# Optimization experiments

Measured on AMD Instinct MI355X. Metric: run time of the kernel, lower is better.

## Reference

```python
import jax, jax.numpy as jnp
import numpy as np

B_, L_, D_MODEL = 2, 2048, 2048
EXPAND = 2
D_IN = EXPAND * D_MODEL            # 4096 intermediate_size
HEADS = 64
HEAD_DIM = D_IN // HEADS           # 64
STATE = 128
NGROUPS = 1
K = 4                              # conv kernel
CONV_DIM = D_IN + 2 * NGROUPS * STATE   # 4352
PROJ = D_IN + CONV_DIM + HEADS          # 8512
CHUNK = 256
EPS = 1e-5


def setup_inputs() -> dict:
    key = jax.random.key(0)
    ks = jax.random.split(key, 4)
    return {
        "hidden_states": jax.random.normal(ks[0], (B_, L_, D_MODEL), jnp.float32),
        "in_proj_w": jax.random.normal(ks[1], (PROJ, D_MODEL), jnp.float32) * 0.02,
        "conv_w": jax.random.normal(ks[2], (CONV_DIM, K), jnp.float32) * 0.2,
        "conv_b": jnp.zeros((CONV_DIM,), jnp.float32),
        "dt_bias": jnp.ones((HEADS,), jnp.float32),
        "A_log": jnp.log(jnp.arange(1, HEADS + 1, dtype=jnp.float32)),
        "D": jnp.ones((HEADS,), jnp.float32),
        "norm_w": jnp.ones((D_IN,), jnp.float32),
        "out_proj_w": jax.random.normal(ks[3], (D_MODEL, D_IN), jnp.float32) * 0.02,
    }


def _segsum(x):
    # x: [..., T] -> lower-triangular segment sums [..., T, T]
    T = x.shape[-1]
    c = jnp.cumsum(x, axis=-1)
    seg = c[..., :, None] - c[..., None, :]
    return jnp.where(jnp.tril(jnp.ones((T, T), bool)), seg, -jnp.inf)


def _ssd(x, dA, Bm, Cm):
    # chunked SSD scan (exact math of the sequential selective scan)
    # x: [b,l,h,p] (already * dt), dA: [b,l,h], Bm/Cm: [b,l,g,n]
    b, l, h, p = x.shape
    n = Bm.shape[-1]
    c = l // CHUNK
    rep = h // Bm.shape[2]
    Bh = jnp.repeat(Bm, rep, axis=2).reshape(b, c, CHUNK, h, n)
    Ch = jnp.repeat(Cm, rep, axis=2).reshape(b, c, CHUNK, h, n)
    x = x.reshape(b, c, CHUNK, h, p)
    dA = dA.reshape(b, c, CHUNK, h).transpose(0, 3, 1, 2)       # [b,h,c,cl]
    dA_cum = jnp.cumsum(dA, axis=-1)
    Lmat = jnp.exp(_segsum(dA))                                  # [b,h,c,cl,cl]
    # intra-chunk (diagonal) contribution
    Y_diag = jnp.einsum('bcthn,bcshn,bhcts,bcshp->bcthp', Ch, Bh, Lmat, x)
    # per-chunk final states
    decay_states = jnp.exp(dA_cum[..., -1:] - dA_cum)            # [b,h,c,cl]
    states = jnp.einsum('bcshn,bhcs,bcshp->bchpn', Bh, decay_states, x)
    # inter-chunk recurrence
    chunk_decay = jnp.exp(_segsum(jnp.pad(dA_cum[..., -1], ((0, 0), (0, 0), (1, 0)))))  # [b,h,c+1,c+1]
    states = jnp.concatenate([jnp.zeros_like(states[:, :1]), states], axis=1)
    prev = jnp.einsum('bhzc,bchpn->bzhpn', chunk_decay, states)[:, :-1]  # state entering each chunk
    Y_off = jnp.einsum('bcthn,bchpn,bhct->bcthp', Ch, prev, jnp.exp(dA_cum))
    return (Y_diag + Y_off).reshape(b, l, h, p)


def reference(hidden_states, in_proj_w, conv_w, conv_b, dt_bias, A_log, D, norm_w, out_proj_w):
    b, l, _ = hidden_states.shape
    proj = hidden_states @ in_proj_w.T                     # [b,l,PROJ]
    gate = proj[..., :D_IN]
    xBC = proj[..., D_IN:D_IN + CONV_DIM]
    dt = proj[..., D_IN + CONV_DIM:]                       # [b,l,H]
    # causal depthwise conv1d (padding=K-1, truncated to seq_len) + silu
    xp = jnp.pad(xBC, ((0, 0), (K - 1, 0), (0, 0)))
    conv = conv_b + sum(conv_w[:, i] * xp[:, i:i + l, :] for i in range(K))
    xBC = jax.nn.silu(conv)
    x = xBC[..., :D_IN].reshape(b, l, HEADS, HEAD_DIM)
    Bm = xBC[..., D_IN:D_IN + NGROUPS * STATE].reshape(b, l, NGROUPS, STATE)
    Cm = xBC[..., D_IN + NGROUPS * STATE:].reshape(b, l, NGROUPS, STATE)
    dt = jax.nn.softplus(dt + dt_bias)                     # time_step_limit=(0,inf): no clamp
    A = -jnp.exp(A_log)                                    # [H]
    y = _ssd(x * dt[..., None], dt * A, Bm, Cm)            # [b,l,H,P]
    y = y + D[None, None, :, None] * x                     # skip term D*x
    y = y.reshape(b, l, D_IN)
    # MambaRMSNormGated: gate then rms-normalize
    hg = y * jax.nn.silu(gate)
    var = jnp.mean(hg * hg, axis=-1, keepdims=True)
    y = hg * jax.lax.rsqrt(var + EPS) * norm_w
    return y @ out_proj_w.T
```

## Files before the change

kernel.cpp:

```cpp
#include <hip/hip_runtime.h>
#include <hip/hip_bf16.h>
#include <cstdio>

#define LQ 2048
#define BB 2
#define BL 4096
#define DMODEL 2048
#define DIN 4096
#define NH 64
#define HD 64
#define NST 128
#define CONVD 4352
#define PROJD 8512
#define PROJ_PAD2 8704
#define PXW 4416
#define CHK 256
#define NCH 8

typedef __attribute__((ext_vector_type(8))) short short8;
typedef __attribute__((ext_vector_type(4))) float f32x4;

__device__ __forceinline__ unsigned short f2bu(float x) {
  __hip_bfloat16 h = __float2bfloat16(x);
  return __builtin_bit_cast(unsigned short, h);
}

__device__ __forceinline__ f32x4 mfma16(short8 a, short8 b, f32x4 c) {
  return __builtin_amdgcn_mfma_f32_16x16x32_bf16(a, b, c, 0, 0, 0);
}

#define GLD16(gptr, lptr)                                                  \
  __builtin_amdgcn_global_load_lds(                                        \
      (const __attribute__((address_space(1))) void*)(gptr),               \
      (__attribute__((address_space(3))) void*)(lptr), 16, 0, 0)

__global__ void k_cast3(const float* __restrict__ s0, unsigned short* __restrict__ d0,
                        long n0,
                        const float* __restrict__ s1, unsigned short* __restrict__ d1,
                        long n1r, long n1t,
                        const float* __restrict__ s2, unsigned short* __restrict__ d2,
                        long n2) {
  const long ntot8 = (n0 + n1t + n2) >> 3;
  long i = (long)blockIdx.x * blockDim.x + threadIdx.x;
  const long stride = (long)gridDim.x * blockDim.x;
  for (; i < ntot8; i += stride) {
    const long e = i << 3;
    const float* src;
    unsigned short* dst;
    long rel, nreal;
    if (e < n0) { src = s0; dst = d0; rel = e; nreal = n0; }
    else if (e < n0 + n1t) { src = s1; dst = d1; rel = e - n0; nreal = n1r; }
    else { src = s2; dst = d2; rel = e - n0 - n1t; nreal = n2; }
    short8 pk;
    if (rel + 8 <= nreal) {
      const f32x4* sp = reinterpret_cast<const f32x4*>(src + rel);
      f32x4 v0 = sp[0], v1 = sp[1];
#pragma unroll
      for (int u = 0; u < 4; u++) {
        pk[u] = (short)f2bu(v0[u]);
        pk[4 + u] = (short)f2bu(v1[u]);
      }
    } else {
#pragma unroll
      for (int u = 0; u < 8; u++)
        pk[u] = (rel + u < nreal) ? (short)f2bu(src[rel + u]) : (short)0;
    }
    *reinterpret_cast<short8*>(dst + rel) = pk;
  }
}

__device__ __forceinline__ short8 rdfrag(const unsigned short (*mp)[64], int rowbase,
                                         int lane, int kh) {
  const int row = rowbase + (lane & 15);
  const int cg = (((kh << 2) + (lane >> 4)) ^ (lane & 7)) << 3;
  return *reinterpret_cast<const short8*>(&mp[row][cg]);
}

template <bool SPLIT>
__global__ __launch_bounds__(512) void k_gemm256(
    const unsigned short* __restrict__ A, const unsigned short* __restrict__ Bw,
    float* __restrict__ C, unsigned short* __restrict__ gateb,
    float* __restrict__ projx, int Nreal, int K) {
  __shared__ unsigned short sh[2][2][256][64];
  const int tid = threadIdx.x;
  const int lane = tid & 63, w = tid >> 6;
  const int wm = w >> 2, wn2 = w & 3;
  const int gx = gridDim.x;
  const int nwg = gx * gridDim.y;
  const int bid = blockIdx.y * gx + blockIdx.x;
  const int qq = nwg >> 3;
  const int swz = (bid & 7) * qq + (bid >> 3);
  const int m0 = (swz / gx) * 256, n0 = (swz % gx) * 256;
  const int srow = tid >> 3;
  const int sdst = (tid & 7) * 8;
  const int ssrc = ((tid & 7) ^ ((tid >> 3) & 7)) * 8;
  const unsigned short* Ab = A + (size_t)m0 * K;
  const unsigned short* Bb = Bw + (size_t)n0 * K;

#define ST(bf, mt, MP, r0, kk)                                             \
  GLD16(MP + (size_t)((r0) + srow) * K + (kk) + ssrc,                      \
        &sh[bf][mt][(r0) + srow][sdst])

  f32x4 acc[8][4] = {};
  const int nt = K >> 6;

  ST(0, 0, Ab, 0, 0);   ST(0, 0, Ab, 128, 0);
  ST(0, 1, Bb, 0, 0);   ST(0, 1, Bb, 64, 0);
  ST(0, 1, Bb, 128, 0); ST(0, 1, Bb, 192, 0);
  ST(0, 0, Ab, 64, 0);  ST(0, 0, Ab, 192, 0);

#define DO_PHASE(P)                                                        \
  {                                                                        \
    const int rb = wm * 128 + (P) * 32;                                    \
    short8 a00 = rdfrag(sh[cur][0], rb, lane, 0);                          \
    short8 a01 = rdfrag(sh[cur][0], rb, lane, 1);                          \
    short8 a10 = rdfrag(sh[cur][0], rb + 16, lane, 0);                     \
    short8 a11 = rdfrag(sh[cur][0], rb + 16, lane, 1);                     \
    __builtin_amdgcn_s_setprio(1);                                         \
    _Pragma("unroll")                                                      \
    for (int nf = 0; nf < 4; nf++) {                                       \
      acc[2 * (P)][nf] = mfma16(a00, bfr[nf][0], acc[2 * (P)][nf]);        \
      acc[2 * (P)][nf] = mfma16(a01, bfr[nf][1], acc[2 * (P)][nf]);        \
      acc[2 * (P) + 1][nf] = mfma16(a10, bfr[nf][0], acc[2 * (P) + 1][nf]);\
      acc[2 * (P) + 1][nf] = mfma16(a11, bfr[nf][1], acc[2 * (P) + 1][nf]);\
    }                                                                      \
    __builtin_amdgcn_s_setprio(0);                                         \
  }

  for (int t = 0; t < nt; ++t) {
    const int cur = t & 1, nxt = cur ^ 1;
    const int kbn = (t + 1) << 6;
    const bool more = (t + 1 < nt);
    asm volatile("s_waitcnt vmcnt(2)" ::: "memory");
    __builtin_amdgcn_s_barrier();
    if (more) { ST(nxt, 0, Ab, 0, kbn); ST(nxt, 0, Ab, 128, kbn); }
    short8 bfr[4][2];
#pragma unroll
    for (int nf = 0; nf < 4; nf++) {
      bfr[nf][0] = rdfrag(sh[cur][1], wn2 * 64 + nf * 16, lane, 0);
      bfr[nf][1] = rdfrag(sh[cur][1], wn2 * 64 + nf * 16, lane, 1);
    }
    DO_PHASE(0)
    __builtin_amdgcn_s_barrier();
    if (more) { ST(nxt, 1, Bb, 0, kbn); ST(nxt, 1, Bb, 64, kbn); }
    DO_PHASE(1)
    if (more) asm volatile("s_waitcnt vmcnt(4)" ::: "memory");
    else      asm volatile("s_waitcnt vmcnt(0)" ::: "memory");
    __builtin_amdgcn_s_barrier();
    if (more) { ST(nxt, 1, Bb, 128, kbn); ST(nxt, 1, Bb, 192, kbn); }
    DO_PHASE(2)
    __builtin_amdgcn_s_barrier();
    if (more) { ST(nxt, 0, Ab, 64, kbn); ST(nxt, 0, Ab, 192, kbn); }
    DO_PHASE(3)
  }
#undef DO_PHASE
#undef ST

#pragma unroll
  for (int mf = 0; mf < 8; mf++) {
    const int row = m0 + wm * 128 + mf * 16 + ((lane >> 4) << 2);
#pragma unroll
    for (int nf = 0; nf < 4; nf++) {
      const int col = n0 + wn2 * 64 + nf * 16 + (lane & 15);
      if (SPLIT) {
        if (col < DIN) {
#pragma unroll
          for (int v = 0; v < 4; v++)
            gateb[(size_t)(row + v) * DIN + col] = f2bu(acc[mf][nf][v]);
        } else if (col < PROJD) {
#pragma unroll
          for (int v = 0; v < 4; v++)
            projx[(size_t)(row + v) * PXW + (col - DIN)] = acc[mf][nf][v];
        }
      } else {
        if (col < Nreal) {
#pragma unroll
          for (int v = 0; v < 4; v++)
            C[(size_t)(row + v) * Nreal + col] = acc[mf][nf][v];
        }
      }
    }
  }
}

__global__ __launch_bounds__(256) void k_gemm_bt(
    const unsigned short* __restrict__ A, const unsigned short* __restrict__ Bw,
    float* __restrict__ C, int Nreal, int K) {
  __shared__ unsigned short lA[128][64];
  __shared__ unsigned short lB[128][64];
  const int tid = threadIdx.x;
  const int lane = tid & 63, w = tid >> 6;
  const int gx = gridDim.x;
  const int nwg = gx * gridDim.y;
  const int bid = blockIdx.y * gx + blockIdx.x;
  const int qq = nwg >> 3;
  const int swz = (bid & 7) * qq + (bid >> 3);
  const int m0 = (swz / gx) * 128, n0 = (swz % gx) * 128;
  const int wr = (w >> 1) * 64, wc = (w & 1) * 64;
  const int sr = tid >> 3;
  const int sdst = (tid & 7) * 8;
  const int ssrc = ((tid & 7) ^ ((tid >> 3) & 7)) * 8;
  f32x4 acc[4][4] = {};
  for (int kb = 0; kb < K; kb += 64) {
#pragma unroll
    for (int i = 0; i < 4; i++) {
      const int r = sr + i * 32;
      GLD16(A + (size_t)(m0 + r) * K + kb + ssrc, &lA[r][sdst]);
      GLD16(Bw + (size_t)(n0 + r) * K + kb + ssrc, &lB[r][sdst]);
    }
    __syncthreads();
#pragma unroll
    for (int kk = 0; kk < 64; kk += 32) {
      short8 af[4], bf[4];
      const int cg = ((((kk >> 3) + (lane >> 4)) ^ (lane & 7)) << 3);
#pragma unroll
      for (int i = 0; i < 4; i++) {
        af[i] = *reinterpret_cast<const short8*>(&lA[wr + i * 16 + (lane & 15)][cg]);
        bf[i] = *reinterpret_cast<const short8*>(&lB[wc + i * 16 + (lane & 15)][cg]);
      }
#pragma unroll
      for (int mi = 0; mi < 4; mi++)
#pragma unroll
        for (int ni = 0; ni < 4; ni++)
          acc[mi][ni] = mfma16(af[mi], bf[ni], acc[mi][ni]);
    }
    __syncthreads();
  }
#pragma unroll
  for (int mi = 0; mi < 4; mi++) {
    const int row = m0 + wr + mi * 16 + ((lane >> 4) << 2);
#pragma unroll
    for (int ni = 0; ni < 4; ni++) {
      const int col = n0 + wc + ni * 16 + (lane & 15);
      if (col < Nreal) {
#pragma unroll
        for (int v = 0; v < 4; v++)
          C[(size_t)(row + v) * Nreal + col] = acc[mi][ni][v];
      }
    }
  }
}

__global__ __launch_bounds__(256) void k_conv_silu(
    const float* __restrict__ projx, const float* __restrict__ cw,
    const float* __restrict__ cb, float* __restrict__ xbc) {
  const int ch = blockIdx.x * 256 + threadIdx.x;
  const int bt = blockIdx.y;
  const int b = bt >> 11, t = bt & 2047;
  float acc = cb[ch];
#pragma unroll
  for (int i = 0; i < 4; i++) {
    int tt = t - 3 + i;
    if (tt >= 0)
      acc += cw[ch * 4 + i] * projx[((size_t)b * LQ + tt) * PXW + ch];
  }
  float o = acc / (1.f + __expf(-acc));
  xbc[(size_t)bt * CONVD + ch] = o;
}

__global__ __launch_bounds__(256) void k_dt(
    const float* __restrict__ projx, const float* __restrict__ dtb,
    const float* __restrict__ alog, float* __restrict__ dtv,
    float* __restrict__ dac) {
  const int bc = blockIdx.x;
  const int b = bc >> 3, c = bc & 7;
  const int h = threadIdx.x & 63, q = threadIdx.x >> 6;
  const float bias = dtb[h];
  const float Ah = -__expf(alog[h]);
  const size_t base = (size_t)b * LQ + c * CHK + q * 64;
  float vals[64];
  float part = 0.f;
#pragma unroll
  for (int j = 0; j < 64; j++) {
    float raw = projx[(base + j) * PXW + CONVD + h] + bias;
    float dt = raw > 20.f ? raw : log1pf(__expf(raw));
    vals[j] = dt;
    dtv[(base + j) * NH + h] = dt;
    part += dt;
  }
  __shared__ float partials[4][64];
  partials[q][h] = part;
  __syncthreads();
  float cum = 0.f;
  for (int qq = 0; qq < q; qq++) cum += partials[qq][h];
  cum *= Ah;
#pragma unroll
  for (int j = 0; j < 64; j++) {
    cum += vals[j] * Ah;
    dac[(base + j) * NH + h] = cum;
  }
}

__global__ __launch_bounds__(256) void k_cb(const float* __restrict__ xbc,
                                            float* __restrict__ cbuf) {
  const int q = blockIdx.x;
  const int bc = blockIdx.y;
  const int b = bc >> 3, c = bc & 7;
  const int qt = q >> 1, qs = q & 1;
  __shared__ unsigned short lC[128][136];
  __shared__ unsigned short lB[128][136];
  const int tid = threadIdx.x, lane = tid & 63, w = tid >> 6;
  {
    int r = tid >> 1, hf = tid & 1;
    size_t rowc = (size_t)b * LQ + c * CHK + qt * 128 + r;
    size_t rowb = (size_t)b * LQ + c * CHK + qs * 128 + r;
    const f32x4* crp = reinterpret_cast<const f32x4*>(
        xbc + rowc * CONVD + DIN + NST + hf * 64);
    const f32x4* brp = reinterpret_cast<const f32x4*>(
        xbc + rowb * CONVD + DIN + hf * 64);
#pragma unroll
    for (int n4 = 0; n4 < 16; n4++) {
      f32x4 vc = crp[n4], vb = brp[n4];
#pragma unroll
      for (int u = 0; u < 4; u++) {
        lC[r][hf * 64 + n4 * 4 + u] = f2bu(vc[u]);
        lB[r][hf * 64 + n4 * 4 + u] = f2bu(vb[u]);
      }
    }
  }
  __syncthreads();
  const int wr = (w >> 1) * 64, wc = (w & 1) * 64;
  f32x4 acc[4][4] = {};
#pragma unroll
  for (int kk = 0; kk < 128; kk += 32) {
    short8 a[4], bb[4];
    const int ko = kk + ((lane >> 4) << 3);
#pragma unroll
    for (int i = 0; i < 4; i++) {
      a[i] = *reinterpret_cast<const short8*>(&lC[wr + i * 16 + (lane & 15)][ko]);
      bb[i] = *reinterpret_cast<const short8*>(&lB[wc + i * 16 + (lane & 15)][ko]);
    }
#pragma unroll
    for (int mi = 0; mi < 4; mi++)
#pragma unroll
      for (int ni = 0; ni < 4; ni++)
        acc[mi][ni] = mfma16(a[mi], bb[ni], acc[mi][ni]);
  }
  float* outp = cbuf + (size_t)bc * (CHK * CHK);
#pragma unroll
  for (int mi = 0; mi < 4; mi++) {
    const int t = qt * 128 + wr + mi * 16 + ((lane >> 4) << 2);
#pragma unroll
    for (int ni = 0; ni < 4; ni++) {
      const int s = qs * 128 + wc + ni * 16 + (lane & 15);
#pragma unroll
      for (int v = 0; v < 4; v++)
        outp[(size_t)(t + v) * CHK + s] = acc[mi][ni][v];
    }
  }
}

__global__ __launch_bounds__(256) void k_diag(
    const float* __restrict__ xbc, const float* __restrict__ dtv,
    const float* __restrict__ dac, const float* __restrict__ cbuf,
    float* __restrict__ y, float* __restrict__ st) {
  const int h = blockIdx.x, c = blockIdx.y, b = blockIdx.z;
  const int cs = c * CHK;
  __shared__ unsigned short lXt[64][136];
  __shared__ unsigned short lBt[128][136];
  __shared__ unsigned short lS[256][40];
  __shared__ float lda[256];
  const int tid = threadIdx.x, lane = tid & 63, w = tid >> 6;
  lda[tid] = dac[((size_t)b * LQ + cs + tid) * NH + h];
  __syncthreads();
  const float dalast = lda[255];
  const float* cbp = cbuf + ((size_t)(b * NCH + c)) * (CHK * CHK);
  const float da_t = lda[tid];
  f32x4 accY[4][4] = {};
  f32x4 accS[4][2] = {};
  const int wn = w * 32;
  const int sl = tid & 127, sub = tid >> 7;
  for (int half = 0; half < 2; half++) {
    {
      const int s = half * 128 + sl;
      const size_t row = (size_t)b * LQ + cs + s;
      const float* xrow = xbc + row * CONVD;
      const float dts = dtv[row * NH + h];
      const float dec = __expf(dalast - lda[s]);
      const f32x4* x4 = reinterpret_cast<const f32x4*>(xrow + h * HD + sub * 32);
#pragma unroll
      for (int p4 = 0; p4 < 8; p4++) {
        f32x4 v = x4[p4];
#pragma unroll
        for (int u = 0; u < 4; u++) lXt[sub * 32 + p4 * 4 + u][sl] = f2bu(v[u] * dts);
      }
      const f32x4* b4 = reinterpret_cast<const f32x4*>(xrow + DIN + sub * 64);
#pragma unroll
      for (int n4 = 0; n4 < 16; n4++) {
        f32x4 v = b4[n4];
#pragma unroll
        for (int u = 0; u < 4; u++) lBt[sub * 64 + n4 * 4 + u][sl] = f2bu(v[u] * dec);
      }
    }
    __syncthreads();
    for (int sb4 = 0; sb4 < 4; sb4++) {
      const int sb = half * 4 + sb4;
      {
        const int t = tid;
        const f32x4* cr = reinterpret_cast<const f32x4*>(cbp + (size_t)t * CHK + sb * 32);
        f32x4 vv[8];
#pragma unroll
        for (int j4 = 0; j4 < 8; j4++) vv[j4] = cr[j4];
#pragma unroll
        for (int g = 0; g < 4; g++) {
          short8 pk;
#pragma unroll
          for (int e = 0; e < 8; e++) {
            const int j = g * 8 + e;
            const int s = sb * 32 + j;
            const float x = vv[j >> 2][j & 3];
            const float val = (s <= t) ? x * __expf(da_t - lda[s]) : 0.f;
            pk[e] = (short)f2bu(val);
          }
          *reinterpret_cast<short8*>(&lS[t][g * 8]) = pk;
        }
      }
      __syncthreads();
      short8 sf[4], xf[4], btf[2];
      const int ko = ((lane >> 4) << 3);
      const int so = sb4 * 32 + ko;
#pragma unroll
      for (int i = 0; i < 4; i++) {
        sf[i] = *reinterpret_cast<const short8*>(&lS[w * 64 + i * 16 + (lane & 15)][ko]);
        xf[i] = *reinterpret_cast<const short8*>(&lXt[i * 16 + (lane & 15)][so]);
      }
#pragma unroll
      for (int i = 0; i < 2; i++)
        btf[i] = *reinterpret_cast<const short8*>(&lBt[wn + i * 16 + (lane & 15)][so]);
#pragma unroll
      for (int mi = 0; mi < 4; mi++)
#pragma unroll
        for (int ni = 0; ni < 4; ni++)
          accY[mi][ni] = mfma16(sf[mi], xf[ni], accY[mi][ni]);
#pragma unroll
      for (int mi = 0; mi < 4; mi++)
#pragma unroll
        for (int nj = 0; nj < 2; nj++)
          accS[mi][nj] = mfma16(xf[mi], btf[nj], accS[mi][nj]);
      __syncthreads();
    }
  }
#pragma unroll
  for (int mi = 0; mi < 4; mi++) {
    const int t = w * 64 + mi * 16 + ((lane >> 4) << 2);
#pragma unroll
    for (int ni = 0; ni < 4; ni++) {
      const int p = ni * 16 + (lane & 15);
#pragma unroll
      for (int v = 0; v < 4; v++)
        y[((size_t)b * LQ + cs + t + v) * DIN + h * HD + p] = accY[mi][ni][v];
    }
  }
  float* stp = st + ((size_t)((b * NCH + c) * NH + h)) * (HD * NST);
#pragma unroll
  for (int mi = 0; mi < 4; mi++) {
    const int p = mi * 16 + ((lane >> 4) << 2);
#pragma unroll
    for (int nj = 0; nj < 2; nj++) {
      const int n = wn + nj * 16 + (lane & 15);
#pragma unroll
      for (int v = 0; v < 4; v++)
        stp[(size_t)(p + v) * NST + n] = accS[mi][nj][v];
    }
  }
}

__global__ void k_scan(const float* __restrict__ st, const float* __restrict__ dac,
                       unsigned short* __restrict__ pv) {
  const int h = blockIdx.x, b = blockIdx.y;
  const int tid = threadIdx.x;
  float P[32];
#pragma unroll
  for (int j = 0; j < 32; j++) P[j] = 0.f;
  for (int c = 0; c < NCH; c++) {
    const size_t base = ((size_t)((b * NCH + c) * NH + h)) * (HD * NST);
#pragma unroll
    for (int j = 0; j < 32; j++) pv[base + tid + 256 * j] = f2bu(P[j]);
    const float d = __expf(dac[((size_t)b * LQ + c * CHK + 255) * NH + h]);
#pragma unroll
    for (int j = 0; j < 32; j++) P[j] = P[j] * d + st[base + tid + 256 * j];
  }
}

__global__ __launch_bounds__(256) void k_off(
    const float* __restrict__ xbc, const float* __restrict__ dac,
    const unsigned short* __restrict__ pv, const float* __restrict__ Dp,
    float* __restrict__ y) {
  const int h = blockIdx.x;
  const int cth = blockIdx.y;
  const int c = cth >> 1, th = cth & 1;
  const int b = blockIdx.z;
  const int cs = c * CHK, t0 = th * 128;
  __shared__ unsigned short lC[128][136];
  __shared__ unsigned short lP[64][136];
  __shared__ float lda[128];
  const int tid = threadIdx.x, lane = tid & 63, w = tid >> 6;
  const int wt = w >> 1, wp = w & 1;
  {
    const int r = tid >> 1, hf = tid & 1;
    const size_t row = (size_t)b * LQ + cs + t0 + r;
    if (hf == 0) lda[r] = dac[row * NH + h];
    const f32x4* cr = reinterpret_cast<const f32x4*>(
        xbc + row * CONVD + DIN + NST + hf * 64);
#pragma unroll
    for (int n4 = 0; n4 < 16; n4++) {
      f32x4 v = cr[n4];
#pragma unroll
      for (int u = 0; u < 4; u++) lC[r][hf * 64 + n4 * 4 + u] = f2bu(v[u]);
    }
  }
  if (tid < 64) {
    const unsigned short* pr =
        pv + ((size_t)((b * NCH + c) * NH + h)) * (HD * NST) + (size_t)tid * NST;
#pragma unroll
    for (int n8 = 0; n8 < 16; n8++)
      *reinterpret_cast<short8*>(&lP[tid][n8 * 8]) =
          *reinterpret_cast<const short8*>(pr + n8 * 8);
  }
  __syncthreads();
  f32x4 acc[4][2] = {};
#pragma unroll
  for (int kk = 0; kk < 128; kk += 32) {
    short8 a[4], bb[2];
    const int ko = kk + ((lane >> 4) << 3);
#pragma unroll
    for (int i = 0; i < 4; i++)
      a[i] = *reinterpret_cast<const short8*>(&lC[wt * 64 + i * 16 + (lane & 15)][ko]);
#pragma unroll
    for (int j = 0; j < 2; j++)
      bb[j] = *reinterpret_cast<const short8*>(&lP[wp * 32 + j * 16 + (lane & 15)][ko]);
#pragma unroll
    for (int mi = 0; mi < 4; mi++)
#pragma unroll
      for (int nj = 0; nj < 2; nj++)
        acc[mi][nj] = mfma16(a[mi], bb[nj], acc[mi][nj]);
  }
  const float Dh = Dp[h];
#pragma unroll
  for (int mi = 0; mi < 4; mi++) {
    const int tl = wt * 64 + mi * 16 + ((lane >> 4) << 2);
#pragma unroll
    for (int nj = 0; nj < 2; nj++) {
      const int p = wp * 32 + nj * 16 + (lane & 15);
#pragma unroll
      for (int v = 0; v < 4; v++) {
        const int tt = tl + v;
        const size_t row = (size_t)b * LQ + cs + t0 + tt;
        const float scale = __expf(lda[tt]);
        const float xval = xbc[row * CONVD + h * HD + p];
        const size_t yi = row * DIN + h * HD + p;
        y[yi] += scale * acc[mi][nj][v] + Dh * xval;
      }
    }
  }
}

__global__ __launch_bounds__(256) void k_gatenorm(
    const float* __restrict__ y, const unsigned short* __restrict__ gateb,
    const float* __restrict__ nw, unsigned short* __restrict__ hgb) {
  const int r = blockIdx.x;
  const int tid = threadIdx.x;
  const float* yr = y + (size_t)r * DIN;
  const unsigned short* gr = gateb + (size_t)r * DIN;
  float hg[16];
  float ss = 0.f;
#pragma unroll
  for (int j = 0; j < 16; j++) {
    const int d = tid + 256 * j;
    const float g = __bfloat162float(__builtin_bit_cast(__hip_bfloat16, gr[d]));
    const float v = yr[d] * (g / (1.f + __expf(-g)));
    hg[j] = v;
    ss += v * v;
  }
#pragma unroll
  for (int o = 32; o > 0; o >>= 1) ss += __shfl_down(ss, o);
  __shared__ float red[4];
  if ((tid & 63) == 0) red[tid >> 6] = ss;
  __syncthreads();
  const float tot = red[0] + red[1] + red[2] + red[3];
  const float scale = rsqrtf(tot / (float)DIN + 1e-5f);
#pragma unroll
  for (int j = 0; j < 16; j++) {
    const int d = tid + 256 * j;
    hgb[(size_t)r * DIN + d] = f2bu(hg[j] * scale * nw[d]);
  }
}

extern "C" void kernel_launch(void* const* d_in, const int* in_sizes, int n_in,
                              void* d_out, int out_size, void* d_ws, size_t ws_size,
                              hipStream_t stream) {
  const float* hidden = (const float*)d_in[0];
  const float* w1 = (const float*)d_in[1];
  const float* cw = (const float*)d_in[2];
  const float* cb = (const float*)d_in[3];
  const float* dtb = (const float*)d_in[4];
  const float* alog = (const float*)d_in[5];
  const float* Dp = (const float*)d_in[6];
  const float* nw = (const float*)d_in[7];
  const float* w2 = (const float*)d_in[8];
  float* out = (float*)d_out;
  char* ws = (char*)d_ws;

  const size_t OFF_GATEB = 0;
  const size_t OFF_XBC = 33554432;
  const size_t OFF_DTV = 104857600;
  const size_t OFF_DAC = 105906176;
  const size_t OFF_CB = 106954752;
  const size_t OFF_Y = 111149056;
  const size_t OFF_ST = 178257920;
  const size_t OFF_PV = 211812352;
  const size_t OFF_PROJX = 111149056;
  const size_t OFF_HB = 183500800;
  const size_t OFF_W1B = 200278016;
  const size_t OFF_W2B = 245366784;
  const size_t OFF_HGB = 33554432;
  const size_t NEED = 262144000;
  if (ws_size < NEED) {
    fprintf(stderr, "WS TOO SMALL: %zu < %zu\n", ws_size, NEED);
    return;
  }
  unsigned short* gateb = (unsigned short*)(ws + OFF_GATEB);
  float* xbc = (float*)(ws + OFF_XBC);
  float* dtv = (float*)(ws + OFF_DTV);
  float* dac = (float*)(ws + OFF_DAC);
  float* cbuf = (float*)(ws + OFF_CB);
  float* y = (float*)(ws + OFF_Y);
  float* st = (float*)(ws + OFF_ST);
  unsigned short* pv = (unsigned short*)(ws + OFF_PV);
  float* projx = (float*)(ws + OFF_PROJX);
  unsigned short* hb = (unsigned short*)(ws + OFF_HB);
  unsigned short* w1b = (unsigned short*)(ws + OFF_W1B);
  unsigned short* w2b = (unsigned short*)(ws + OFF_W2B);
  unsigned short* hgb = (unsigned short*)(ws + OFF_HGB);

  k_cast3<<<4096, 256, 0, stream>>>(hidden, hb, (long)BL * DMODEL,
                                    w1, w1b, (long)PROJD * DMODEL,
                                    (long)PROJ_PAD2 * DMODEL,
                                    w2, w2b, (long)DMODEL * DIN);
  k_gemm256<true><<<dim3(PROJ_PAD2 / 256, BL / 256), 512, 0, stream>>>(
      hb, w1b, nullptr, gateb, projx, PROJD, DMODEL);
  k_conv_silu<<<dim3(17, BL), 256, 0, stream>>>(projx, cw, cb, xbc);
  k_dt<<<16, 256, 0, stream>>>(projx, dtb, alog, dtv, dac);
  k_cb<<<dim3(4, 16), 256, 0, stream>>>(xbc, cbuf);
  k_diag<<<dim3(NH, NCH, BB), 256, 0, stream>>>(xbc, dtv, dac, cbuf, y, st);
  k_scan<<<dim3(NH, BB), 256, 0, stream>>>(st, dac, pv);
  k_off<<<dim3(NH, NCH * 2, BB), 256, 0, stream>>>(xbc, dac, pv, Dp, y);
  k_gatenorm<<<BL, 256, 0, stream>>>(y, gateb, nw, hgb);
  k_gemm_bt<<<dim3(DMODEL / 128, BL / 128), 256, 0, stream>>>(
      hgb, w2b, out, DMODEL, DIN);
}
```

Measured before the change: 630.7 us.

## Store conv output in bf16 and skip masked blocks in diagonal score build

The conv+silu output buffer xbc is now stored as bf16 rather than fp32, which halves its write and read traffic in conv, cb, diag and off kernels, and lets C/B tiles be copied straight into LDS without conversion. In k_diag the decay-weighted score build now branches per 32-column block. Fully masked blocks are zero-filled, and strictly-lower blocks factor the exponent into a per-row term times a precomputed per-column term. This removes most per-element exp calls. Rounding x to bf16 before the D skip term and the dt scaling adds a small precision loss.

```diff
diff --git a/kernel.cpp b/kernel.cpp
--- a/kernel.cpp
+++ b/kernel.cpp
@@ -23,6 +23,10 @@
 __device__ __forceinline__ unsigned short f2bu(float x) {
   __hip_bfloat16 h = __float2bfloat16(x);
   return __builtin_bit_cast(unsigned short, h);
+}
+
+__device__ __forceinline__ float b2f(unsigned short u) {
+  return __bfloat162float(__builtin_bit_cast(__hip_bfloat16, u));
 }
 
 __device__ __forceinline__ f32x4 mfma16(short8 a, short8 b, f32x4 c) {
@@ -243,7 +247,7 @@
 
 __global__ __launch_bounds__(256) void k_conv_silu(
     const float* __restrict__ projx, const float* __restrict__ cw,
-    const float* __restrict__ cb, float* __restrict__ xbc) {
+    const float* __restrict__ cb, unsigned short* __restrict__ xbc) {
   const int ch = blockIdx.x * 256 + threadIdx.x;
   const int bt = blockIdx.y;
   const int b = bt >> 11, t = bt & 2047;
@@ -255,7 +259,7 @@
       acc += cw[ch * 4 + i] * projx[((size_t)b * LQ + tt) * PXW + ch];
   }
   float o = acc / (1.f + __expf(-acc));
-  xbc[(size_t)bt * CONVD + ch] = o;
+  xbc[(size_t)bt * CONVD + ch] = f2bu(o);
 }
 
 __global__ __launch_bounds__(256) void k_dt(
@@ -291,7 +295,7 @@
   }
 }
 
-__global__ __launch_bounds__(256) void k_cb(const float* __restrict__ xbc,
+__global__ __launch_bounds__(256) void k_cb(const unsigned short* __restrict__ xbc,
                                             float* __restrict__ cbuf) {
   const int q = blockIdx.x;
   const int bc = blockIdx.y;
@@ -304,18 +308,14 @@
     int r = tid >> 1, hf = tid & 1;
     size_t rowc = (size_t)b * LQ + c * CHK + qt * 128 + r;
     size_t rowb = (size_t)b * LQ + c * CHK + qs * 128 + r;
-    const f32x4* crp = reinterpret_cast<const f32x4*>(
-        xbc + rowc * CONVD + DIN + NST + hf * 64);
-    const f32x4* brp = reinterpret_cast<const f32x4*>(
-        xbc + rowb * CONVD + DIN + hf * 64);
-#pragma unroll
-    for (int n4 = 0; n4 < 16; n4++) {
-      f32x4 vc = crp[n4], vb = brp[n4];
-#pragma unroll
-      for (int u = 0; u < 4; u++) {
-        lC[r][hf * 64 + n4 * 4 + u] = f2bu(vc[u]);
-        lB[r][hf * 64 + n4 * 4 + u] = f2bu(vb[u]);
-      }
+    const unsigned short* crp = xbc + rowc * CONVD + DIN + NST + hf * 64;
+    const unsigned short* brp = xbc + rowb * CONVD + DIN + hf * 64;
+#pragma unroll
+    for (int n8 = 0; n8 < 8; n8++) {
+      *reinterpret_cast<short8*>(&lC[r][hf * 64 + n8 * 8]) =
+          *reinterpret_cast<const short8*>(crp + n8 * 8);
+      *reinterpret_cast<short8*>(&lB[r][hf * 64 + n8 * 8]) =
+          *reinterpret_cast<const short8*>(brp + n8 * 8);
     }
   }
   __syncthreads();
@@ -351,7 +351,7 @@
 }
 
 __global__ __launch_bounds__(256) void k_diag(
-    const float* __restrict__ xbc, const float* __restrict__ dtv,
+    const unsigned short* __restrict__ xbc, const float* __restrict__ dtv,
     const float* __restrict__ dac, const float* __restrict__ cbuf,
     float* __restrict__ y, float* __restrict__ st) {
   const int h = blockIdx.x, c = blockIdx.y, b = blockIdx.z;
@@ -360,9 +360,11 @@
   __shared__ unsigned short lBt[128][136];
   __shared__ unsigned short lS[256][40];
   __shared__ float lda[256];
+  __shared__ float lesE[256];
   const int tid = threadIdx.x, lane = tid & 63, w = tid >> 6;
   lda[tid] = dac[((size_t)b * LQ + cs + tid) * NH + h];
   __syncthreads();
+  lesE[tid] = __expf(lda[tid | 31] - lda[tid]);
   const float dalast = lda[255];
   const float* cbp = cbuf + ((size_t)(b * NCH + c)) * (CHK * CHK);
   const float da_t = lda[tid];
@@ -374,22 +376,22 @@
     {
       const int s = half * 128 + sl;
       const size_t row = (size_t)b * LQ + cs + s;
-      const float* xrow = xbc + row * CONVD;
+      const unsigned short* xrow = xbc + row * CONVD;
       const float dts = dtv[row * NH + h];
       const float dec = __expf(dalast - lda[s]);
-      const f32x4* x4 = reinterpret_cast<const f32x4*>(xrow + h * HD + sub * 32);
-#pragma unroll
-      for (int p4 = 0; p4 < 8; p4++) {
-        f32x4 v = x4[p4];
-#pragma unroll
-        for (int u = 0; u < 4; u++) lXt[sub * 32 + p4 * 4 + u][sl] = f2bu(v[u] * dts);
-      }
-      const f32x4* b4 = reinterpret_cast<const f32x4*>(xrow + DIN + sub * 64);
-#pragma unroll
-      for (int n4 = 0; n4 < 16; n4++) {
-        f32x4 v = b4[n4];
-#pragma unroll
-        for (int u = 0; u < 4; u++) lBt[sub * 64 + n4 * 4 + u][sl] = f2bu(v[u] * dec);
+#pragma unroll
+      for (int g = 0; g < 4; g++) {
+        short8 xv = *reinterpret_cast<const short8*>(xrow + h * HD + sub * 32 + g * 8);
+#pragma unroll
+        for (int u = 0; u < 8; u++)
+          lXt[sub * 32 + g * 8 + u][sl] = f2bu(b2f((unsigned short)xv[u]) * dts);
+      }
+#pragma unroll
+      for (int g = 0; g < 8; g++) {
+        short8 bv = *reinterpret_cast<const short8*>(xrow + DIN + sub * 64 + g * 8);
+#pragma unroll
+        for (int u = 0; u < 8; u++)
+          lBt[sub * 64 + g * 8 + u][sl] = f2bu(b2f((unsigned short)bv[u]) * dec);
       }
     }
     __syncthreads();
@@ -397,22 +399,46 @@
       const int sb = half * 4 + sb4;
       {
         const int t = tid;
-        const f32x4* cr = reinterpret_cast<const f32x4*>(cbp + (size_t)t * CHK + sb * 32);
-        f32x4 vv[8];
-#pragma unroll
-        for (int j4 = 0; j4 < 8; j4++) vv[j4] = cr[j4];
-#pragma unroll
-        for (int g = 0; g < 4; g++) {
-          short8 pk;
-#pragma unroll
-          for (int e = 0; e < 8; e++) {
-            const int j = g * 8 + e;
-            const int s = sb * 32 + j;
-            const float x = vv[j >> 2][j & 3];
-            const float val = (s <= t) ? x * __expf(da_t - lda[s]) : 0.f;
-            pk[e] = (short)f2bu(val);
+        const int tb = t >> 5;
+        if (tb > sb) {
+          const float et = __expf(da_t - lda[sb * 32 + 31]);
+          const f32x4* cr = reinterpret_cast<const f32x4*>(cbp + (size_t)t * CHK + sb * 32);
+          f32x4 vv[8];
+#pragma unroll
+          for (int j4 = 0; j4 < 8; j4++) vv[j4] = cr[j4];
+#pragma unroll
+          for (int g = 0; g < 4; g++) {
+            short8 pk;
+#pragma unroll
+            for (int e = 0; e < 8; e++) {
+              const int j = g * 8 + e;
+              pk[e] = (short)f2bu(vv[j >> 2][j & 3] * et * lesE[sb * 32 + j]);
+            }
+            *reinterpret_cast<short8*>(&lS[t][g * 8]) = pk;
           }
-          *reinterpret_cast<short8*>(&lS[t][g * 8]) = pk;
+        } else if (tb == sb) {
+          const f32x4* cr = reinterpret_cast<const f32x4*>(cbp + (size_t)t * CHK + sb * 32);
+          f32x4 vv[8];
+#pragma unroll
+          for (int j4 = 0; j4 < 8; j4++) vv[j4] = cr[j4];
+          const int tl = t & 31;
+#pragma unroll
+          for (int g = 0; g < 4; g++) {
+            short8 pk;
+#pragma unroll
+            for (int e = 0; e < 8; e++) {
+              const int j = g * 8 + e;
+              float val = (j <= tl)
+                  ? vv[j >> 2][j & 3] * __expf(da_t - lda[sb * 32 + j]) : 0.f;
+              pk[e] = (short)f2bu(val);
+            }
+            *reinterpret_cast<short8*>(&lS[t][g * 8]) = pk;
+          }
+        } else {
+          short8 z = {};
+#pragma unroll
+          for (int g = 0; g < 4; g++)
+            *reinterpret_cast<short8*>(&lS[tid][g * 8]) = z;
         }
       }
       __syncthreads();
@@ -483,7 +509,7 @@
 }
 
 __global__ __launch_bounds__(256) void k_off(
-    const float* __restrict__ xbc, const float* __restrict__ dac,
+    const unsigned short* __restrict__ xbc, const float* __restrict__ dac,
     const unsigned short* __restrict__ pv, const float* __restrict__ Dp,
     float* __restrict__ y) {
   const int h = blockIdx.x;
@@ -500,14 +526,11 @@
     const int r = tid >> 1, hf = tid & 1;
     const size_t row = (size_t)b * LQ + cs + t0 + r;
     if (hf == 0) lda[r] = dac[row * NH + h];
-    const f32x4* cr = reinterpret_cast<const f32x4*>(
-        xbc + row * CONVD + DIN + NST + hf * 64);
-#pragma unroll
-    for (int n4 = 0; n4 < 16; n4++) {
-      f32x4 v = cr[n4];
-#pragma unroll
-      for (int u = 0; u < 4; u++) lC[r][hf * 64 + n4 * 4 + u] = f2bu(v[u]);
-    }
+    const unsigned short* cr = xbc + row * CONVD + DIN + NST + hf * 64;
+#pragma unroll
+    for (int n8 = 0; n8 < 8; n8++)
+      *reinterpret_cast<short8*>(&lC[r][hf * 64 + n8 * 8]) =
+          *reinterpret_cast<const short8*>(cr + n8 * 8);
   }
   if (tid < 64) {
     const unsigned short* pr =
@@ -547,7 +570,7 @@
         const int tt = tl + v;
         const size_t row = (size_t)b * LQ + cs + t0 + tt;
         const float scale = __expf(lda[tt]);
-        const float xval = xbc[row * CONVD + h * HD + p];
+        const float xval = b2f(xbc[row * CONVD + h * HD + p]);
         const size_t yi = row * DIN + h * HD + p;
         y[yi] += scale * acc[mi][nj][v] + Dh * xval;
       }
@@ -567,7 +590,7 @@
 #pragma unroll
   for (int j = 0; j < 16; j++) {
     const int d = tid + 256 * j;
-    const float g = __bfloat162float(__builtin_bit_cast(__hip_bfloat16, gr[d]));
+    const float g = b2f(gr[d]);
     const float v = yr[d] * (g / (1.f + __expf(-g)));
     hg[j] = v;
     ss += v * v;
@@ -620,7 +643,7 @@
     return;
   }
   unsigned short* gateb = (unsigned short*)(ws + OFF_GATEB);
-  float* xbc = (float*)(ws + OFF_XBC);
+  unsigned short* xbc = (unsigned short*)(ws + OFF_XBC);
   float* dtv = (float*)(ws + OFF_DTV);
   float* dac = (float*)(ws + OFF_DAC);
   float* cbuf = (float*)(ws + OFF_CB);
```

Measured after the change: 551.4 us. 1.14x faster.
